# Optimization experiments

Measured on AMD Instinct MI355X. Metric: run time of the kernel, lower is better.

The kernel has to match this reference:

```python
import jax, jax.numpy as jnp
import numpy as np

N = 64000            # total nodes (64 graphs x 1000 nodes)
E = 1048576          # edges (~16 avg degree)
NB_NODES = 1000
NUM_GRAPHS = 64
F_IN, H1, H2, H3, OUT = 128, 256, 256, 128, 64


def setup_inputs() -> dict:
    key = jax.random.key(0)
    ks = jax.random.split(key, 12)
    x = jax.random.normal(ks[0], (N, F_IN), dtype=jnp.float32)
    # random edges within each graph: pick graph per edge, then local src/dst
    g = jax.random.randint(ks[1], (E,), 0, NUM_GRAPHS)
    src = g * NB_NODES + jax.random.randint(ks[2], (E,), 0, NB_NODES)
    dst = g * NB_NODES + jax.random.randint(ks[3], (E,), 0, NB_NODES)
    edge_index = jnp.stack([src, dst]).astype(jnp.int64)
    batch = (jnp.arange(N) // NB_NODES).astype(jnp.int64)  # sorted graph ids
    def glorot(k, fan_in, fan_out):
        s = jnp.sqrt(6.0 / (fan_in + fan_out))
        return jax.random.uniform(k, (fan_in, fan_out), jnp.float32, -s, s)
    return {
        "x": x, "edge_index": edge_index, "batch": batch,
        "W1": glorot(ks[4], F_IN, H1), "b1": jnp.zeros((H1,), jnp.float32),
        "W2": glorot(ks[5], H1, H2),   "b2": jnp.zeros((H2,), jnp.float32),
        "W3": glorot(ks[6], H2, H3),   "b3": jnp.zeros((H3,), jnp.float32),
        "Wfc": glorot(ks[7], H3 * NB_NODES, OUT),
        "bfc": jnp.zeros((OUT,), jnp.float32),
    }


def _gcn_norm(edge_index, n):
    # add self-loops, symmetric normalization D^-1/2 (A+I) D^-1/2
    loop = jnp.arange(n, dtype=edge_index.dtype)
    src = jnp.concatenate([edge_index[0], loop])
    dst = jnp.concatenate([edge_index[1], loop])
    deg = jax.ops.segment_sum(jnp.ones_like(src, jnp.float32), dst, num_segments=n)
    dinv = 1.0 / jnp.sqrt(deg)  # deg >= 1 thanks to self-loops
    norm = dinv[src] * dinv[dst]
    return src, dst, norm


def _gcn_layer(h, W, b, src, dst, norm, n):
    hl = h @ W                                   # [N, H]
    msg = hl[src] * norm[:, None]                # gather + scale
    agg = jax.ops.segment_sum(msg, dst, num_segments=n)  # scatter-add
    return agg + b


def reference(x, edge_index, batch, W1, b1, W2, b2, W3, b3, Wfc, bfc):
    n = x.shape[0]
    src, dst, norm = _gcn_norm(edge_index, n)
    h = jnp.tanh(_gcn_layer(x, W1, b1, src, dst, norm, n))
    h = jnp.tanh(_gcn_layer(h, W2, b2, src, dst, norm, n))
    h = jnp.tanh(_gcn_layer(h, W3, b3, src, dst, norm, n))
    # batch is sorted with equal graph sizes -> the per-graph loop/concat
    # in the original is exactly a reshape to [num_graphs, nodes*H3]
    h_concat = h.reshape(NUM_GRAPHS, NB_NODES * H3)
    return h_concat @ Wfc + bfc
```

## Files before the change

kernel.cpp:

```cpp
#include <hip/hip_runtime.h>
#include <math.h>

#define N_NODES 64000
#define N_EDGES 1048576
#define NB 1000
#define NG 64
#define NOUT 64
#define FC_SPLIT 500
#define BK_CAP 18000

typedef __attribute__((ext_vector_type(8))) short bfrag;
typedef __attribute__((ext_vector_type(4))) float f32x4;
typedef __attribute__((ext_vector_type(2))) float f32x2;

__device__ inline float bf2f(unsigned short u) {
    union { unsigned int i; float f; } x; x.i = ((unsigned int)u) << 16; return x.f;
}
__device__ inline float bflo(unsigned int u) {
    union { unsigned int i; float f; } x; x.i = u << 16; return x.f;
}
__device__ inline float bfhi(unsigned int u) {
    union { unsigned int i; float f; } x; x.i = u & 0xffff0000u; return x.f;
}
__device__ inline f32x2 upk(unsigned int u) {
    f32x2 r; r.x = bflo(u); r.y = bfhi(u); return r;
}
__device__ inline unsigned short f2bf(float f) {
    union { float f; unsigned int i; } x; x.f = f;
    return (unsigned short)((x.i + 0x7FFFu + ((x.i >> 16) & 1u)) >> 16);
}
__device__ inline float tanh_fast(float x) {
    float e = __expf(2.0f * x);
    return fmaf(-2.0f, __builtin_amdgcn_rcpf(e + 1.0f), 1.0f);
}
__device__ inline int swz32(int row, int g) { return g ^ (row & 7) ^ (g >> 3); }
__device__ inline int swz16(int row, int g) { return g ^ (row & 7) ^ (g >> 3); }

__device__ inline void gload_lds16(const unsigned short* g, unsigned short* l) {
    __builtin_amdgcn_global_load_lds(
        (const __attribute__((address_space(1))) void*)g,
        (__attribute__((address_space(3))) void*)l, 16, 0, 0);
}


__global__ __launch_bounds__(256) void k_bucket(const int* __restrict__ src,
                                                const int* __restrict__ dst,
                                                int* __restrict__ gcnt,
                                                unsigned int* __restrict__ bucket) {
    __shared__ int lcnt[64];
    __shared__ int lbase[64];
    __shared__ int lcur[64];
    int t = threadIdx.x;
    int e0 = blockIdx.x * 4096;
    if (t < 64) { lcnt[t] = 0; lcur[t] = 0; }
    __syncthreads();
    for (int i = t; i < 4096; i += 256) {
        int d = dst[e0 + i];
        int g = d / NB;
        atomicAdd(&lcnt[g], 1);
    }
    __syncthreads();
    if (t < 64) lbase[t] = atomicAdd(&gcnt[t], lcnt[t]);
    __syncthreads();
    for (int i = t; i < 4096; i += 256) {
        int d = dst[e0 + i];
        int s = src[e0 + i];
        int g = d / NB;
        int pos = atomicAdd(&lcur[g], 1);
        unsigned int packed = ((unsigned int)(d - g * NB) << 10) | (unsigned int)(s - g * NB);
        bucket[(size_t)g * BK_CAP + lbase[g] + pos] = packed;
    }
}

__global__ __launch_bounds__(1024) void k_build(const int* __restrict__ gcnt,
                                                const unsigned int* __restrict__ bucket,
                                                int* __restrict__ rowptr,
                                                int* __restrict__ rowend,
                                                float* __restrict__ dinv,
                                                unsigned short* __restrict__ colp) {
    __shared__ int ind[1024];
    __shared__ int tmp[1024];
    int t = threadIdx.x;
    int g = blockIdx.x;
    int cnt = gcnt[g];
    size_t base = (size_t)g * BK_CAP;
    ind[t] = 0;
    __syncthreads();
    for (int i = t; i < cnt; i += 1024) {
        unsigned int p = bucket[base + i];
        atomicAdd(&ind[p >> 10], 1);
    }
    __syncthreads();
    int deg = ind[t];
    if (t < NB) dinv[g * NB + t] = rsqrtf((float)(deg + 1));
    tmp[t] = deg;
    __syncthreads();
    for (int off = 1; off < 1024; off <<= 1) {
        int o = (t >= off) ? tmp[t - off] : 0;
        __syncthreads();
        tmp[t] += o;
        __syncthreads();
    }
    int excl = tmp[t] - deg;
    if (t < NB) {
        rowptr[g * NB + t] = (int)base + excl;
        rowend[g * NB + t] = (int)base + excl + deg;
    }
    ind[t] = excl;
    __syncthreads();
    for (int i = t; i < cnt; i += 1024) {
        unsigned int p = bucket[base + i];
        int dl = p >> 10;
        int pos = atomicAdd(&ind[dl], 1);
        colp[base + pos] = (unsigned short)(p & 1023u);
    }
}


__global__ void k_cast_scale(const float* __restrict__ in, const float* __restrict__ dinv,
                             unsigned short* __restrict__ out) {
    int i = (blockIdx.x * blockDim.x + threadIdx.x) * 4;
    float d = dinv[i >> 7];
    float4 v = *(const float4*)(in + i);
    union { unsigned short s[4]; uint2 u; } o;
    o.s[0] = f2bf(v.x * d); o.s[1] = f2bf(v.y * d);
    o.s[2] = f2bf(v.z * d); o.s[3] = f2bf(v.w * d);
    *(uint2*)(out + i) = o.u;
}

__global__ void k_wt(const float* __restrict__ W, unsigned short* __restrict__ Wt,
                     int K, int N) {
    int i = blockIdx.x * 256 + threadIdx.x;
    if (i < K * N) {
        int n = i / K, k = i % K;
        Wt[i] = f2bf(W[k * N + n]);
    }
}


template <int H, bool TANH>
__global__ void k_agg(const unsigned short* __restrict__ hs, unsigned short* __restrict__ op,
                      const int* __restrict__ rowptr, const int* __restrict__ rowend,
                      const unsigned short* __restrict__ col,
                      const float* __restrict__ dinv, const float* __restrict__ bias) {
    constexpr int VEC = H / 64;
    int lane = threadIdx.x & 63;
    int b = blockIdx.x;
    int c = b & 7;
    int j = b >> 3;
    int g = c + 8 * (j / 250);
    int chunk = j % 250;
    int v = g * NB + chunk * 4 + (threadIdx.x >> 6);
    const unsigned short* gb = hs + (size_t)g * NB * H;
    f32x2 a0, a1;
    {
        const unsigned short* r = hs + (size_t)v * H + lane * VEC;
        if (VEC == 2) {
            a0 = upk(*(const unsigned int*)r);
        } else {
            uint2 u = *(const uint2*)r;
            a0 = upk(u.x); a1 = upk(u.y);
        }
    }
    int beg = rowptr[v], end = rowend[v];
    for (int e0 = beg; e0 < end; e0 += 64) {
        int me = e0 + lane;
        int s = (me < end) ? (int)col[me] : 0;
        int cnt = min(64, end - e0);
        int i = 0;
        for (; i + 8 <= cnt; i += 8) {
            int sx[8];
#pragma unroll
            for (int q = 0; q < 8; ++q) sx[q] = __builtin_amdgcn_readlane(s, i + q);
            if (VEC == 2) {
                unsigned int u[8];
#pragma unroll
                for (int q = 0; q < 8; ++q)
                    u[q] = *(const unsigned int*)(gb + (size_t)sx[q] * H + lane * 2);
#pragma unroll
                for (int q = 0; q < 8; ++q) a0 += upk(u[q]);
            } else {
                uint2 u[8];
#pragma unroll
                for (int q = 0; q < 8; ++q)
                    u[q] = *(const uint2*)(gb + (size_t)sx[q] * H + lane * 4);
#pragma unroll
                for (int q = 0; q < 8; ++q) { a0 += upk(u[q].x); a1 += upk(u[q].y); }
            }
        }
        for (; i + 4 <= cnt; i += 4) {
            int sx[4];
#pragma unroll
            for (int q = 0; q < 4; ++q) sx[q] = __builtin_amdgcn_readlane(s, i + q);
            if (VEC == 2) {
                unsigned int u[4];
#pragma unroll
                for (int q = 0; q < 4; ++q)
                    u[q] = *(const unsigned int*)(gb + (size_t)sx[q] * H + lane * 2);
#pragma unroll
                for (int q = 0; q < 4; ++q) a0 += upk(u[q]);
            } else {
                uint2 u[4];
#pragma unroll
                for (int q = 0; q < 4; ++q)
                    u[q] = *(const uint2*)(gb + (size_t)sx[q] * H + lane * 4);
#pragma unroll
                for (int q = 0; q < 4; ++q) { a0 += upk(u[q].x); a1 += upk(u[q].y); }
            }
        }
        for (; i < cnt; ++i) {
            int ss = __builtin_amdgcn_readlane(s, i);
            if (VEC == 2) {
                a0 += upk(*(const unsigned int*)(gb + (size_t)ss * H + lane * 2));
            } else {
                uint2 u = *(const uint2*)(gb + (size_t)ss * H + lane * 4);
                a0 += upk(u.x); a1 += upk(u.y);
            }
        }
    }
    float dv = dinv[v];
    float acc[4];
    acc[0] = a0.x; acc[1] = a0.y;
    if (VEC == 4) { acc[2] = a1.x; acc[3] = a1.y; }
    if (TANH) {
#pragma unroll
        for (int q = 0; q < VEC; ++q) acc[q] = tanh_fast(acc[q] * dv + bias[lane * VEC + q]);
    } else {
#pragma unroll
        for (int q = 0; q < VEC; ++q) acc[q] *= dv;
    }
    unsigned short* o = op + (size_t)v * H + lane * VEC;
    if (VEC == 2) {
        union { unsigned short s[2]; unsigned int u; } pk;
        pk.s[0] = f2bf(acc[0]); pk.s[1] = f2bf(acc[1]);
        *(unsigned int*)o = pk.u;
    } else {
        union { unsigned short s[4]; uint2 u; } pk;
        pk.s[0] = f2bf(acc[0]); pk.s[1] = f2bf(acc[1]);
        pk.s[2] = f2bf(acc[2]); pk.s[3] = f2bf(acc[3]);
        *(uint2*)o = pk.u;
    }
}


__global__ __launch_bounds__(256, 2) void k_gemm1(const unsigned short* __restrict__ A,
                                                  const unsigned short* __restrict__ W1t,
                                                  const float* __restrict__ b1,
                                                  const float* __restrict__ dinv,
                                                  unsigned short* __restrict__ C) {
    constexpr int K = 128, N = 256;
    __shared__ unsigned short at[2][64 * 128];
    int t = threadIdx.x;
    int w = t >> 6, l = t & 63;
    int lm = l & 15, lq = l >> 4;
    int n0 = w * 64;
    int row0 = lq * 4;
    int tile0 = blockIdx.x * 2;

    {
        const unsigned short* Ab = A + (size_t)tile0 * 64 * K;
#pragma unroll
        for (int q = 0; q < 4; ++q) {
            int rbase = w * 16 + q * 4;
            int row = rbase + (l >> 4);
            int g = swz16(row, l & 15);
            gload_lds16(Ab + (size_t)row * K + g * 8, &at[0][rbase * K]);
        }
    }
    bfrag B1[16];
    {
        const unsigned short* Bb = W1t + (size_t)(n0 + lm) * K + lq * 8;
#pragma unroll
        for (int j = 0; j < 4; ++j)
#pragma unroll
            for (int it = 0; it < 4; ++it)
                B1[j * 4 + it] = *(const bfrag*)(Bb + (size_t)j * 16 * K + it * 32);
    }
    float bj[4];
#pragma unroll
    for (int j = 0; j < 4; ++j) bj[j] = b1[n0 + j * 16 + lm];

#pragma unroll
    for (int tt = 0; tt < 2; ++tt) {
        int m0 = (tile0 + tt) * 64;
        if (tt == 0) {
            const unsigned short* Ab = A + (size_t)(tile0 + 1) * 64 * K;
#pragma unroll
            for (int q = 0; q < 4; ++q) {
                int rbase = w * 16 + q * 4;
                int row = rbase + (l >> 4);
                int g = swz16(row, l & 15);
                gload_lds16(Ab + (size_t)row * K + g * 8, &at[1][rbase * K]);
            }
            asm volatile("s_waitcnt vmcnt(4)\n\ts_barrier" ::: "memory");
        } else {
            asm volatile("s_waitcnt vmcnt(0)\n\ts_barrier" ::: "memory");
        }
        const unsigned short* buf = at[tt];
        f32x4 acc[4][4] = {};
#pragma unroll
        for (int it = 0; it < 4; ++it) {
            bfrag af[4];
            int gidx = it * 4 + lq;
#pragma unroll
            for (int i = 0; i < 4; ++i) {
                int row = i * 16 + lm;
                af[i] = *(const bfrag*)&buf[row * K + swz16(row, gidx) * 8];
            }
#pragma unroll
            for (int i = 0; i < 4; ++i)
#pragma unroll
                for (int j = 0; j < 4; ++j)
                    acc[i][j] = __builtin_amdgcn_mfma_f32_16x16x32_bf16(af[i], B1[j * 4 + it], acc[i][j], 0, 0, 0);
        }
        float drow[4][4];
#pragma unroll
        for (int i = 0; i < 4; ++i)
#pragma unroll
            for (int r = 0; r < 4; ++r) drow[i][r] = dinv[m0 + i * 16 + row0 + r];
#pragma unroll
        for (int i = 0; i < 4; ++i)
#pragma unroll
            for (int j = 0; j < 4; ++j)
#pragma unroll
                for (int r = 0; r < 4; ++r) {
                    float v = tanh_fast(acc[i][j][r] + bj[j]) * drow[i][r];
                    C[(size_t)(m0 + i * 16 + row0 + r) * N + n0 + j * 16 + lm] = f2bf(v);
                }
    }
}


__global__ __launch_bounds__(256, 2) void k_gemm23(const unsigned short* __restrict__ A,
                                                   const unsigned short* __restrict__ W2t,
                                                   const float* __restrict__ b2,
                                                   const unsigned short* __restrict__ W3t,
                                                   const float* __restrict__ dinv,
                                                   unsigned short* __restrict__ C) {
    constexpr int K = 256, N3 = 128;
    __shared__ unsigned short at[2][64 * 256];
    int t = threadIdx.x;
    int w = t >> 6, l = t & 63;
    int lm = l & 15, lq = l >> 4;
    int n0 = w * 64;
    int row0 = lq * 4;
    int tile0 = blockIdx.x * 2;

    {
        const unsigned short* Ab = A + (size_t)tile0 * 64 * K;
#pragma unroll
        for (int q = 0; q < 8; ++q) {
            int rbase = w * 16 + q * 2;
            int row = rbase + (l >> 5);
            int g = swz32(row, l & 31);
            gload_lds16(Ab + (size_t)row * K + g * 8, &at[0][rbase * K]);
        }
    }
    bfrag B1[32];
    {
        const unsigned short* Bb = W2t + (size_t)(n0 + lm) * K + lq * 8;
#pragma unroll
        for (int j = 0; j < 4; ++j)
#pragma unroll
            for (int it = 0; it < 8; ++it)
                B1[j * 8 + it] = *(const bfrag*)(Bb + (size_t)j * 16 * K + it * 32);
    }
    float bj[4];
#pragma unroll
    for (int j = 0; j < 4; ++j) bj[j] = b2[n0 + j * 16 + lm];

#pragma unroll
    for (int tt = 0; tt < 2; ++tt) {
        int m0 = (tile0 + tt) * 64;
        if (tt == 0) {
            const unsigned short* Ab = A + (size_t)(tile0 + 1) * 64 * K;
#pragma unroll
            for (int q = 0; q < 8; ++q) {
                int rbase = w * 16 + q * 2;
                int row = rbase + (l >> 5);
                int g = swz32(row, l & 31);
                gload_lds16(Ab + (size_t)row * K + g * 8, &at[1][rbase * K]);
            }
            asm volatile("s_waitcnt vmcnt(8)\n\ts_barrier" ::: "memory");
        } else {
            asm volatile("s_waitcnt vmcnt(0)\n\ts_barrier" ::: "memory");
        }
        unsigned short* buf = at[tt];
        f32x4 acc[4][4] = {};
#pragma unroll
        for (int it = 0; it < 8; ++it) {
            bfrag af[4];
            int gidx = it * 4 + lq;
#pragma unroll
            for (int i = 0; i < 4; ++i) {
                int row = i * 16 + lm;
                af[i] = *(const bfrag*)&buf[row * 256 + swz32(row, gidx) * 8];
            }
#pragma unroll
            for (int i = 0; i < 4; ++i)
#pragma unroll
                for (int j = 0; j < 4; ++j)
                    acc[i][j] = __builtin_amdgcn_mfma_f32_16x16x32_bf16(af[i], B1[j * 8 + it], acc[i][j], 0, 0, 0);
        }
        asm volatile("s_waitcnt lgkmcnt(0)\n\ts_barrier" ::: "memory");
#pragma unroll
        for (int i = 0; i < 4; ++i)
#pragma unroll
            for (int j = 0; j < 4; ++j) {
                int colb = n0 + j * 16 + lm;
                int gidx = colb >> 3, off = colb & 7;
#pragma unroll
                for (int r = 0; r < 4; ++r) {
                    int row = i * 16 + row0 + r;
                    buf[row * 256 + swz32(row, gidx) * 8 + off] =
                        f2bf(tanh_fast(acc[i][j][r] + bj[j]));
                }
            }
        asm volatile("s_waitcnt lgkmcnt(0)\n\ts_barrier" ::: "memory");
        {
            f32x4 acc2[4][2] = {};
            int n3 = w * 32;
            const unsigned short* Bb = W3t + (size_t)(n3 + lm) * K + lq * 8;
            bfrag bfb[2][2];
#pragma unroll
            for (int j = 0; j < 2; ++j) bfb[0][j] = *(const bfrag*)(Bb + (size_t)j * 16 * K);
#pragma unroll
            for (int it = 0; it < 8; ++it) {
                int ks = it * 32, pc = it & 1;
                if (it + 1 < 8) {
#pragma unroll
                    for (int j = 0; j < 2; ++j)
                        bfb[pc ^ 1][j] = *(const bfrag*)(Bb + (size_t)j * 16 * K + ks + 32);
                }
                bfrag af[4];
                int gidx = it * 4 + lq;
#pragma unroll
                for (int i = 0; i < 4; ++i) {
                    int row = i * 16 + lm;
                    af[i] = *(const bfrag*)&buf[row * 256 + swz32(row, gidx) * 8];
                }
#pragma unroll
                for (int i = 0; i < 4; ++i)
#pragma unroll
                    for (int j = 0; j < 2; ++j)
                        acc2[i][j] = __builtin_amdgcn_mfma_f32_16x16x32_bf16(af[i], bfb[pc][j], acc2[i][j], 0, 0, 0);
            }
            float drow[4][4];
#pragma unroll
            for (int i = 0; i < 4; ++i)
#pragma unroll
                for (int r = 0; r < 4; ++r) drow[i][r] = dinv[m0 + i * 16 + row0 + r];
#pragma unroll
            for (int i = 0; i < 4; ++i)
#pragma unroll
                for (int j = 0; j < 2; ++j)
#pragma unroll
                    for (int r = 0; r < 4; ++r)
                        C[(size_t)(m0 + i * 16 + row0 + r) * N3 + n3 + j * 16 + lm] =
                            f2bf(acc2[i][j][r] * drow[i][r]);
        }
    }
}


__global__ void k_fc(const unsigned short* __restrict__ A, const float* __restrict__ B,
                     float* __restrict__ part) {
    __shared__ float As[16][68];
    __shared__ float Bs[16][68];
    const int KROW = NB * 128;
    int t = threadIdx.x;
    int tx = t & 15, ty = t >> 4;
    int k0b = blockIdx.x * 256;
    float acc[4][4] = {};
    for (int k0 = k0b; k0 < k0b + 256; k0 += 16) {
        int arow = t >> 2, ak = (t & 3) << 2;
        uint2 ua = *(const uint2*)(A + (size_t)arow * KROW + k0 + ak);
        As[ak + 0][arow] = bflo(ua.x);
        As[ak + 1][arow] = bfhi(ua.x);
        As[ak + 2][arow] = bflo(ua.y);
        As[ak + 3][arow] = bfhi(ua.y);
        int bk = t >> 4, bn4 = (t & 15) << 2;
        *(float4*)&Bs[bk][bn4] = *(const float4*)(B + (size_t)(k0 + bk) * NOUT + bn4);
        __syncthreads();
#pragma unroll
        for (int kk = 0; kk < 16; ++kk) {
            float4 a = *(const float4*)&As[kk][ty << 2];
            float4 b = *(const float4*)&Bs[kk][tx << 2];
            acc[0][0] += a.x * b.x; acc[0][1] += a.x * b.y; acc[0][2] += a.x * b.z; acc[0][3] += a.x * b.w;
            acc[1][0] += a.y * b.x; acc[1][1] += a.y * b.y; acc[1][2] += a.y * b.z; acc[1][3] += a.y * b.w;
            acc[2][0] += a.z * b.x; acc[2][1] += a.z * b.y; acc[2][2] += a.z * b.z; acc[2][3] += a.z * b.w;
            acc[3][0] += a.w * b.x; acc[3][1] += a.w * b.y; acc[3][2] += a.w * b.z; acc[3][3] += a.w * b.w;
        }
        __syncthreads();
    }
    float* po = part + (size_t)blockIdx.x * (NG * NOUT);
#pragma unroll
    for (int i = 0; i < 4; ++i) {
        float4 r;
        r.x = acc[i][0]; r.y = acc[i][1]; r.z = acc[i][2]; r.w = acc[i][3];
        *(float4*)&po[((ty << 2) + i) * NOUT + (tx << 2)] = r;
    }
}

__global__ void k_fc_reduce(const float* __restrict__ part, const float* __restrict__ bfc,
                            float* __restrict__ out) {
    int i = blockIdx.x * blockDim.x + threadIdx.x;
    float s = bfc[i & 63];
    for (int b = 0; b < FC_SPLIT; ++b) s += part[(size_t)b * (NG * NOUT) + i];
    out[i] = s;
}


static inline size_t align256(size_t x) { return (x + 255) & ~(size_t)255; }

extern "C" void kernel_launch(void* const* d_in, const int* in_sizes, int n_in,
                              void* d_out, int out_size, void* d_ws, size_t ws_size,
                              hipStream_t stream) {
    const float* x   = (const float*)d_in[0];
    const int*   ei  = (const int*)d_in[1];
    const int*   src = ei;
    const int*   dst = ei + N_EDGES;
    const float* W1  = (const float*)d_in[3];
    const float* b1  = (const float*)d_in[4];
    const float* W2  = (const float*)d_in[5];
    const float* b2  = (const float*)d_in[6];
    const float* W3  = (const float*)d_in[7];
    const float* b3  = (const float*)d_in[8];
    const float* Wfc = (const float*)d_in[9];
    const float* bfc = (const float*)d_in[10];
    float* out = (float*)d_out;

    char* w = (char*)d_ws;
    unsigned short* P0 = (unsigned short*)w; w += align256((size_t)N_NODES * 256 * 2);
    unsigned short* P1 = (unsigned short*)w; w += align256((size_t)N_NODES * 256 * 2);
    unsigned short* P2 = (unsigned short*)w; w += align256((size_t)N_NODES * 256 * 2);
    int* rowptr = (int*)w;      w += align256((size_t)N_NODES * 4);
    int* rowend = (int*)w;      w += align256((size_t)N_NODES * 4);
    float* dinv = (float*)w;    w += align256((size_t)N_NODES * 4);
    int* gcnt = (int*)w;        w += align256((size_t)NG * 4);
    unsigned int* bucket = (unsigned int*)w; w += align256((size_t)NG * BK_CAP * 4);
    unsigned short* colp = (unsigned short*)w; w += align256((size_t)NG * BK_CAP * 2);
    float* fcpart = (float*)w;  w += align256((size_t)FC_SPLIT * NG * NOUT * 4);
    unsigned short* W1t = (unsigned short*)w; w += align256((size_t)128 * 256 * 2);
    unsigned short* W2t = (unsigned short*)w; w += align256((size_t)256 * 256 * 2);
    unsigned short* W3t = (unsigned short*)w; w += align256((size_t)256 * 128 * 2);

    hipMemsetAsync(gcnt, 0, (size_t)NG * 4, stream);
    k_bucket<<<N_EDGES / 4096, 256, 0, stream>>>(src, dst, gcnt, bucket);
    k_build<<<NG, 1024, 0, stream>>>(gcnt, bucket, rowptr, rowend, dinv, colp);

    k_cast_scale<<<(N_NODES * 128 / 4) / 256, 256, 0, stream>>>(x, dinv, P0);
    k_wt<<<(128 * 256 + 255) / 256, 256, 0, stream>>>(W1, W1t, 128, 256);
    k_wt<<<(256 * 256 + 255) / 256, 256, 0, stream>>>(W2, W2t, 256, 256);
    k_wt<<<(256 * 128 + 255) / 256, 256, 0, stream>>>(W3, W3t, 256, 128);

    k_agg<128, false><<<N_NODES / 4, 256, 0, stream>>>(P0, P1, rowptr, rowend, colp, dinv, nullptr);
    k_gemm1<<<N_NODES / 128, 256, 0, stream>>>(P1, W1t, b1, dinv, P2);

    k_agg<256, false><<<N_NODES / 4, 256, 0, stream>>>(P2, P0, rowptr, rowend, colp, dinv, nullptr);
    k_gemm23<<<N_NODES / 128, 256, 0, stream>>>(P0, W2t, b2, W3t, dinv, P1);

    k_agg<128, true><<<N_NODES / 4, 256, 0, stream>>>(P1, P0, rowptr, rowend, colp, dinv, b3);

    k_fc<<<FC_SPLIT, 256, 0, stream>>>(P0, Wfc, fcpart);
    k_fc_reduce<<<NG * NOUT / 256, 256, 0, stream>>>(fcpart, bfc, out);
}
```

Baseline: 333.1 us.

## Process one 64-row tile per block in GEMM kernels, dropping double buffering

The GEMM kernels now handle a single 64-row tile per block instead of two, which doubles the grid and halves LDS use. The in-block prefetch of the second tile is removed. In gemm23, the W3 fragment loads are hoisted before the first GEMM and deepened to a 4-slot ring with prefetch distance 2. The aim is more blocks and better occupancy, at the cost of reloading the weight fragments into registers twice as often.

```diff
diff --git a/kernel.cpp b/kernel.cpp
--- a/kernel.cpp
+++ b/kernel.cpp
@@ -249,22 +249,22 @@
                                                   const float* __restrict__ dinv,
                                                   unsigned short* __restrict__ C) {
     constexpr int K = 128, N = 256;
-    __shared__ unsigned short at[2][64 * 128];
+    __shared__ unsigned short at[64 * 128];
     int t = threadIdx.x;
     int w = t >> 6, l = t & 63;
     int lm = l & 15, lq = l >> 4;
     int n0 = w * 64;
     int row0 = lq * 4;
-    int tile0 = blockIdx.x * 2;
+    int m0 = blockIdx.x * 64;
 
     {
-        const unsigned short* Ab = A + (size_t)tile0 * 64 * K;
+        const unsigned short* Ab = A + (size_t)m0 * K;
 #pragma unroll
         for (int q = 0; q < 4; ++q) {
             int rbase = w * 16 + q * 4;
             int row = rbase + (l >> 4);
             int g = swz16(row, l & 15);
-            gload_lds16(Ab + (size_t)row * K + g * 8, &at[0][rbase * K]);
+            gload_lds16(Ab + (size_t)row * K + g * 8, &at[rbase * K]);
         }
     }
     bfrag B1[16];
@@ -280,54 +280,38 @@
 #pragma unroll
     for (int j = 0; j < 4; ++j) bj[j] = b1[n0 + j * 16 + lm];
 
-#pragma unroll
-    for (int tt = 0; tt < 2; ++tt) {
-        int m0 = (tile0 + tt) * 64;
-        if (tt == 0) {
-            const unsigned short* Ab = A + (size_t)(tile0 + 1) * 64 * K;
-#pragma unroll
-            for (int q = 0; q < 4; ++q) {
-                int rbase = w * 16 + q * 4;
-                int row = rbase + (l >> 4);
-                int g = swz16(row, l & 15);
-                gload_lds16(Ab + (size_t)row * K + g * 8, &at[1][rbase * K]);
-            }
-            asm volatile("s_waitcnt vmcnt(4)\n\ts_barrier" ::: "memory");
-        } else {
-            asm volatile("s_waitcnt vmcnt(0)\n\ts_barrier" ::: "memory");
-        }
-        const unsigned short* buf = at[tt];
-        f32x4 acc[4][4] = {};
-#pragma unroll
-        for (int it = 0; it < 4; ++it) {
-            bfrag af[4];
-            int gidx = it * 4 + lq;
-#pragma unroll
-            for (int i = 0; i < 4; ++i) {
-                int row = i * 16 + lm;
-                af[i] = *(const bfrag*)&buf[row * K + swz16(row, gidx) * 8];
-            }
-#pragma unroll
-            for (int i = 0; i < 4; ++i)
-#pragma unroll
-                for (int j = 0; j < 4; ++j)
-                    acc[i][j] = __builtin_amdgcn_mfma_f32_16x16x32_bf16(af[i], B1[j * 4 + it], acc[i][j], 0, 0, 0);
-        }
-        float drow[4][4];
+    asm volatile("s_waitcnt vmcnt(0)\n\ts_barrier" ::: "memory");
+
+    f32x4 acc[4][4] = {};
+#pragma unroll
+    for (int it = 0; it < 4; ++it) {
+        bfrag af[4];
+        int gidx = it * 4 + lq;
+#pragma unroll
+        for (int i = 0; i < 4; ++i) {
+            int row = i * 16 + lm;
+            af[i] = *(const bfrag*)&at[row * K + swz16(row, gidx) * 8];
+        }
 #pragma unroll
         for (int i = 0; i < 4; ++i)
 #pragma unroll
-            for (int r = 0; r < 4; ++r) drow[i][r] = dinv[m0 + i * 16 + row0 + r];
-#pragma unroll
-        for (int i = 0; i < 4; ++i)
-#pragma unroll
             for (int j = 0; j < 4; ++j)
-#pragma unroll
-                for (int r = 0; r < 4; ++r) {
-                    float v = tanh_fast(acc[i][j][r] + bj[j]) * drow[i][r];
-                    C[(size_t)(m0 + i * 16 + row0 + r) * N + n0 + j * 16 + lm] = f2bf(v);
-                }
-    }
+                acc[i][j] = __builtin_amdgcn_mfma_f32_16x16x32_bf16(af[i], B1[j * 4 + it], acc[i][j], 0, 0, 0);
+    }
+    float drow[4][4];
+#pragma unroll
+    for (int i = 0; i < 4; ++i)
+#pragma unroll
+        for (int r = 0; r < 4; ++r) drow[i][r] = dinv[m0 + i * 16 + row0 + r];
+#pragma unroll
+    for (int i = 0; i < 4; ++i)
+#pragma unroll
+        for (int j = 0; j < 4; ++j)
+#pragma unroll
+            for (int r = 0; r < 4; ++r) {
+                float v = tanh_fast(acc[i][j][r] + bj[j]) * drow[i][r];
+                C[(size_t)(m0 + i * 16 + row0 + r) * N + n0 + j * 16 + lm] = f2bf(v);
+            }
 }
 
 
@@ -338,22 +322,24 @@
                                                    const float* __restrict__ dinv,
                                                    unsigned short* __restrict__ C) {
     constexpr int K = 256, N3 = 128;
-    __shared__ unsigned short at[2][64 * 256];
+    __shared__ unsigned short at[64 * 256];
     int t = threadIdx.x;
     int w = t >> 6, l = t & 63;
     int lm = l & 15, lq = l >> 4;
     int n0 = w * 64;
     int row0 = lq * 4;
-    int tile0 = blockIdx.x * 2;
+    int m0 = blockIdx.x * 64;
+    int n3 = w * 32;
+    const unsigned short* B3b = W3t + (size_t)(n3 + lm) * K + lq * 8;
 
     {
-        const unsigned short* Ab = A + (size_t)tile0 * 64 * K;
+        const unsigned short* Ab = A + (size_t)m0 * K;
 #pragma unroll
         for (int q = 0; q < 8; ++q) {
             int rbase = w * 16 + q * 2;
             int row = rbase + (l >> 5);
             int g = swz32(row, l & 31);
-            gload_lds16(Ab + (size_t)row * K + g * 8, &at[0][rbase * K]);
+            gload_lds16(Ab + (size_t)row * K + g * 8, &at[rbase * K]);
         }
     }
     bfrag B1[32];
@@ -365,100 +351,84 @@
             for (int it = 0; it < 8; ++it)
                 B1[j * 8 + it] = *(const bfrag*)(Bb + (size_t)j * 16 * K + it * 32);
     }
+    bfrag bfb[4][2];
+#pragma unroll
+    for (int p = 0; p < 2; ++p)
+#pragma unroll
+        for (int j = 0; j < 2; ++j)
+            bfb[p][j] = *(const bfrag*)(B3b + (size_t)j * 16 * K + p * 32);
     float bj[4];
 #pragma unroll
     for (int j = 0; j < 4; ++j) bj[j] = b2[n0 + j * 16 + lm];
 
-#pragma unroll
-    for (int tt = 0; tt < 2; ++tt) {
-        int m0 = (tile0 + tt) * 64;
-        if (tt == 0) {
-            const unsigned short* Ab = A + (size_t)(tile0 + 1) * 64 * K;
-#pragma unroll
-            for (int q = 0; q < 8; ++q) {
-                int rbase = w * 16 + q * 2;
-                int row = rbase + (l >> 5);
-                int g = swz32(row, l & 31);
-                gload_lds16(Ab + (size_t)row * K + g * 8, &at[1][rbase * K]);
-            }
-            asm volatile("s_waitcnt vmcnt(8)\n\ts_barrier" ::: "memory");
-        } else {
-            asm volatile("s_waitcnt vmcnt(0)\n\ts_barrier" ::: "memory");
-        }
-        unsigned short* buf = at[tt];
-        f32x4 acc[4][4] = {};
+    asm volatile("s_waitcnt vmcnt(0)\n\ts_barrier" ::: "memory");
+
+    f32x4 acc[4][4] = {};
+#pragma unroll
+    for (int it = 0; it < 8; ++it) {
+        bfrag af[4];
+        int gidx = it * 4 + lq;
+#pragma unroll
+        for (int i = 0; i < 4; ++i) {
+            int row = i * 16 + lm;
+            af[i] = *(const bfrag*)&at[row * 256 + swz32(row, gidx) * 8];
+        }
+#pragma unroll
+        for (int i = 0; i < 4; ++i)
+#pragma unroll
+            for (int j = 0; j < 4; ++j)
+                acc[i][j] = __builtin_amdgcn_mfma_f32_16x16x32_bf16(af[i], B1[j * 8 + it], acc[i][j], 0, 0, 0);
+    }
+    asm volatile("s_waitcnt lgkmcnt(0)\n\ts_barrier" ::: "memory");
+#pragma unroll
+    for (int i = 0; i < 4; ++i)
+#pragma unroll
+        for (int j = 0; j < 4; ++j) {
+            int colb = n0 + j * 16 + lm;
+            int gidx = colb >> 3, off = colb & 7;
+#pragma unroll
+            for (int r = 0; r < 4; ++r) {
+                int row = i * 16 + row0 + r;
+                at[row * 256 + swz32(row, gidx) * 8 + off] =
+                    f2bf(tanh_fast(acc[i][j][r] + bj[j]));
+            }
+        }
+    asm volatile("s_waitcnt lgkmcnt(0)\n\ts_barrier" ::: "memory");
+    {
+        f32x4 acc2[4][2] = {};
 #pragma unroll
         for (int it = 0; it < 8; ++it) {
+            if (it + 2 < 8) {
+#pragma unroll
+                for (int j = 0; j < 2; ++j)
+                    bfb[(it + 2) & 3][j] = *(const bfrag*)(B3b + (size_t)j * 16 * K + (it + 2) * 32);
+            }
             bfrag af[4];
             int gidx = it * 4 + lq;
 #pragma unroll
             for (int i = 0; i < 4; ++i) {
                 int row = i * 16 + lm;
-                af[i] = *(const bfrag*)&buf[row * 256 + swz32(row, gidx) * 8];
+                af[i] = *(const bfrag*)&at[row * 256 + swz32(row, gidx) * 8];
             }
 #pragma unroll
             for (int i = 0; i < 4; ++i)
 #pragma unroll
-                for (int j = 0; j < 4; ++j)
-                    acc[i][j] = __builtin_amdgcn_mfma_f32_16x16x32_bf16(af[i], B1[j * 8 + it], acc[i][j], 0, 0, 0);
-        }
-        asm volatile("s_waitcnt lgkmcnt(0)\n\ts_barrier" ::: "memory");
+                for (int j = 0; j < 2; ++j)
+                    acc2[i][j] = __builtin_amdgcn_mfma_f32_16x16x32_bf16(af[i], bfb[it & 3][j], acc2[i][j], 0, 0, 0);
+        }
+        float drow[4][4];
 #pragma unroll
         for (int i = 0; i < 4; ++i)
 #pragma unroll
-            for (int j = 0; j < 4; ++j) {
-                int colb = n0 + j * 16 + lm;
-                int gidx = colb >> 3, off = colb & 7;
-#pragma unroll
-                for (int r = 0; r < 4; ++r) {
-                    int row = i * 16 + row0 + r;
-                    buf[row * 256 + swz32(row, gidx) * 8 + off] =
-                        f2bf(tanh_fast(acc[i][j][r] + bj[j]));
-                }
-            }
-        asm volatile("s_waitcnt lgkmcnt(0)\n\ts_barrier" ::: "memory");
-        {
-            f32x4 acc2[4][2] = {};
-            int n3 = w * 32;
-            const unsigned short* Bb = W3t + (size_t)(n3 + lm) * K + lq * 8;
-            bfrag bfb[2][2];
-#pragma unroll
-            for (int j = 0; j < 2; ++j) bfb[0][j] = *(const bfrag*)(Bb + (size_t)j * 16 * K);
-#pragma unroll
-            for (int it = 0; it < 8; ++it) {
-                int ks = it * 32, pc = it & 1;
-                if (it + 1 < 8) {
-#pragma unroll
-                    for (int j = 0; j < 2; ++j)
-                        bfb[pc ^ 1][j] = *(const bfrag*)(Bb + (size_t)j * 16 * K + ks + 32);
-                }
-                bfrag af[4];
-                int gidx = it * 4 + lq;
-#pragma unroll
-                for (int i = 0; i < 4; ++i) {
-                    int row = i * 16 + lm;
-                    af[i] = *(const bfrag*)&buf[row * 256 + swz32(row, gidx) * 8];
-                }
-#pragma unroll
-                for (int i = 0; i < 4; ++i)
-#pragma unroll
-                    for (int j = 0; j < 2; ++j)
-                        acc2[i][j] = __builtin_amdgcn_mfma_f32_16x16x32_bf16(af[i], bfb[pc][j], acc2[i][j], 0, 0, 0);
-            }
-            float drow[4][4];
-#pragma unroll
-            for (int i = 0; i < 4; ++i)
-#pragma unroll
-                for (int r = 0; r < 4; ++r) drow[i][r] = dinv[m0 + i * 16 + row0 + r];
-#pragma unroll
-            for (int i = 0; i < 4; ++i)
-#pragma unroll
-                for (int j = 0; j < 2; ++j)
-#pragma unroll
-                    for (int r = 0; r < 4; ++r)
-                        C[(size_t)(m0 + i * 16 + row0 + r) * N3 + n3 + j * 16 + lm] =
-                            f2bf(acc2[i][j][r] * drow[i][r]);
-        }
+            for (int r = 0; r < 4; ++r) drow[i][r] = dinv[m0 + i * 16 + row0 + r];
+#pragma unroll
+        for (int i = 0; i < 4; ++i)
+#pragma unroll
+            for (int j = 0; j < 2; ++j)
+#pragma unroll
+                for (int r = 0; r < 4; ++r)
+                    C[(size_t)(m0 + i * 16 + row0 + r) * N3 + n3 + j * 16 + lm] =
+                        f2bf(acc2[i][j][r] * drow[i][r]);
     }
 }
 
@@ -555,10 +525,10 @@
     k_wt<<<(256 * 128 + 255) / 256, 256, 0, stream>>>(W3, W3t, 256, 128);
 
     k_agg<128, false><<<N_NODES / 4, 256, 0, stream>>>(P0, P1, rowptr, rowend, colp, dinv, nullptr);
-    k_gemm1<<<N_NODES / 128, 256, 0, stream>>>(P1, W1t, b1, dinv, P2);
+    k_gemm1<<<N_NODES / 64, 256, 0, stream>>>(P1, W1t, b1, dinv, P2);
 
     k_agg<256, false><<<N_NODES / 4, 256, 0, stream>>>(P2, P0, rowptr, rowend, colp, dinv, nullptr);
-    k_gemm23<<<N_NODES / 128, 256, 0, stream>>>(P0, W2t, b2, W3t, dinv, P1);
+    k_gemm23<<<N_NODES / 64, 256, 0, stream>>>(P0, W2t, b2, W3t, dinv, P1);
 
     k_agg<128, true><<<N_NODES / 4, 256, 0, stream>>>(P1, P0, rowptr, rowend, colp, dinv, b3);
 
```

Result: slower. 342.4 us (+2.8%).
